# Performance work log

Hardware: AMD Instinct MI355X
Metric: run time of the kernel (lower is better)

The kernel has to match this reference:

```python
import jax, jax.numpy as jnp
import numpy as np


def _conv(x, w, b):
    # NCHW conv, SAME padding for odd kernel, stride 1
    pad = (w.shape[2] - 1) // 2
    y = jax.lax.conv_general_dilated(
        x, w, window_strides=(1, 1), padding=[(pad, pad), (pad, pad)],
        dimension_numbers=('NCHW', 'OIHW', 'NCHW'))
    return y + b[None, :, None, None]


def _cell(x, h, c, m, p):
    # one TransGRU cell step; x:[B,Cin,H,W], h/c/m:[B,hc,H,W]
    A = _conv(jnp.concatenate([x, h], axis=1), p['w_rzo'], p['b_rzo'])   # [B,3hc,H,W]
    Bm = _conv(jnp.concatenate([x, m], axis=1), p['w_rz'], p['b_rz'])    # [B,2hc,H,W]
    decay_h = jnp.exp(-p['td_h'])[None]          # (1,hc,1,1)
    decay_m = jnp.exp(-p['td_m'])[None]
    gate = jax.nn.sigmoid(p['tg'])[None]
    Ar, Az, Ao = jnp.split(A, 3, axis=1)
    Br, Bz = jnp.split(Bm, 2, axis=1)
    r = jax.nn.sigmoid(Ar * gate + h * decay_h)
    z = jax.nn.sigmoid(Az * gate + h * decay_h)
    o = jax.nn.sigmoid(Ao)
    xr = jax.nn.sigmoid(Br * gate + m * decay_m)
    xz = jax.nn.sigmoid(Bz * gate + m * decay_m)
    gc = jnp.tanh(_conv(jnp.concatenate([x, r * c], axis=1), p['w_h'], p['b_h']))
    gm = jnp.tanh(_conv(jnp.concatenate([x, xr * m], axis=1), p['w_h'], p['b_h']))
    c_new = z * c + (1 - z) * gc
    m_new = xz * m + (1 - xz) * gm
    h_new = o * jnp.tanh(_conv(jnp.concatenate([c_new, m_new], axis=1), p['w_o'], p['b_o']))
    return h_new, c_new, m_new, (r, z, xr, xz, c_new, m_new, gc, gm, o)


def _forward(x, params, attention_size):
    B, T, _, H, W = x.shape
    L = len(params)
    hcs = [p['w_rzo'].shape[0] // 3 for p in params]
    hc_last = hcs[-1]
    dtype = x.dtype
    init_states = tuple(
        tuple(jnp.zeros((B, hc, H, W), dtype) for _ in range(3)) for hc in hcs)
    init_gates = tuple(jnp.zeros((B, hc_last, H, W), dtype) for _ in range(9))

    def step(carry, xt):
        states, _ = carry
        inp = xt
        m = states[-1][2]  # layer 0 reads m from last layer of previous step
        new_states = []
        gates = None
        for l in range(L):
            h, c, _own_m = states[l]
            inp, cn, mn, gates = _cell(inp, h, c, m, params[l])
            new_states.append((inp, cn, mn))
            m = mn  # next layer reads m just produced by this layer
        return (tuple(new_states), gates), inp

    (final_states, gates), hs = jax.lax.scan(
        step, (init_states, init_gates), jnp.swapaxes(x, 0, 1))
    # gates from last layer at final step (matches torch leaking loop vars)
    r, z, xr, xz, c, m, gc, gm, o = gates
    q = ((r + xr + c + gc) * 0.25).reshape(B, hc_last, H * W)
    k = ((r + xr + m + gm) * 0.25).reshape(B, hc_last, H * W)
    v = jnp.swapaxes(hs, 0, 1).reshape(B, T, hc_last, H * W)
    scale = 1.0 / float(np.sqrt(attention_size))
    attn = jax.nn.softmax(jnp.einsum('bcn,bdn->bcd', q, k) * scale, axis=-1)
    out = jnp.einsum('bcd,btdn->btcn', attn, v).reshape(B, T, hc_last, H, W)
    return out


def setup_inputs() -> dict:
    key = jax.random.key(0)
    ks = jax.random.split(key, 32)
    d = {'x': jax.random.normal(ks[0], (4, 8, 16, 64, 64), jnp.float32)}
    specs = {
        'w_rzo0': (192, 80, 3, 3), 'b_rzo0': (192,), 'w_rz0': (128, 80, 3, 3),
        'b_rz0': (128,), 'w_h0': (64, 80, 3, 3), 'b_h0': (64,),
        'w_o0': (64, 128, 1, 1), 'b_o0': (64,), 'td_h0': (64, 1, 1),
        'td_m0': (64, 1, 1), 'tg0': (64, 1, 1),
        'w_rzo1': (192, 128, 3, 3), 'b_rzo1': (192,), 'w_rz1': (128, 128, 3, 3),
        'b_rz1': (128,), 'w_h1': (64, 128, 3, 3), 'b_h1': (64,),
        'w_o1': (64, 128, 1, 1), 'b_o1': (64,), 'td_h1': (64, 1, 1),
        'td_m1': (64, 1, 1), 'tg1': (64, 1, 1),
    }
    for i, (name, shp) in enumerate(specs.items()):
        d[name] = jax.random.normal(ks[i + 1], shp, jnp.float32) * 0.05
    d['attention_size'] = 4096
    return d


def reference(x, w_rzo0, b_rzo0, w_rz0, b_rz0, w_h0, b_h0, w_o0, b_o0,
              td_h0, td_m0, tg0, w_rzo1, b_rzo1, w_rz1, b_rz1, w_h1, b_h1,
              w_o1, b_o1, td_h1, td_m1, tg1, attention_size):
    params = [
        dict(w_rzo=w_rzo0, b_rzo=b_rzo0, w_rz=w_rz0, b_rz=b_rz0, w_h=w_h0,
             b_h=b_h0, w_o=w_o0, b_o=b_o0, td_h=td_h0, td_m=td_m0, tg=tg0),
        dict(w_rzo=w_rzo1, b_rzo=b_rzo1, w_rz=w_rz1, b_rz=b_rz1, w_h=w_h1,
             b_h=b_h1, w_o=w_o1, b_o=b_o1, td_h=td_h1, td_m=td_m1, tg=tg1),
    ]
    return _forward(x, params, attention_size)
```

## Files before the change

kernel.cpp:

```cpp
#include <hip/hip_runtime.h>
#include <math.h>

#define HWN 4096
#define Bn 4
#define Tn 8

typedef __attribute__((ext_vector_type(8))) _Float16 f16x8;
typedef __attribute__((ext_vector_type(4))) float floatx4;

__device__ __forceinline__ float sigmoidf_(float v) { return 1.f / (1.f + expf(-v)); }

__device__ __forceinline__ void split8(const float* vv, f16x8* hi, f16x8* lo) {
#pragma unroll
    for (int j = 0; j < 8; ++j) {
        _Float16 h = (_Float16)vv[j];
        (*hi)[j] = h;
        (*lo)[j] = (_Float16)(vv[j] - (float)h);
    }
}

__global__ __launch_bounds__(256) void prep_w_kernel(
    const float* __restrict__ W, _Float16* __restrict__ dst,
    int Ctot, int Cout, int nch, int KK)
{
    const int ncog = Cout >> 4;
    const long total = (long)KK * nch * ncog * 512;
    for (long i = (long)blockIdx.x * 256 + threadIdx.x; i < total;
         i += (long)gridDim.x * 256) {
        int j    = (int)(i & 7);
        int lane = (int)((i >> 3) & 63);
        long r   = i >> 9;
        int f = (int)(r % ncog); r /= ncog;
        int c = (int)(r % nch);  r /= nch;
        int kk = (int)r;
        int co = f * 16 + (lane & 15);
        int ci = c * 32 + (lane >> 4) * 8 + j;
        float v = (ci < Ctot) ? W[((long)co * Ctot + ci) * KK + kk] : 0.f;
        _Float16 hi = (_Float16)v;
        dst[i]         = hi;
        dst[total + i] = (_Float16)(v - (float)hi);
    }
}

__global__ __launch_bounds__(256) void prep_x_kernel(
    const float* __restrict__ x, float* __restrict__ xcl)
{
    const int i = blockIdx.x * 256 + threadIdx.x;
    const int px = i & 4095;
    const int t  = (i >> 12) & 7;
    const int b  = i >> 15;
    float* d = xcl + (((long)t * Bn + b) * HWN + px) * 16;
#pragma unroll
    for (int ch = 0; ch < 16; ++ch)
        d[ch] = x[((long)(b * 8 + t) * 16 + ch) * HWN + px];
}

template<int EPI, int NF>
__global__ __launch_bounds__(256) void conv3m(
    const float* __restrict__ in1, int C1,
    const float* __restrict__ in2a, const float* __restrict__ in2b,
    int Ctot, int nch,
    const _Float16* __restrict__ wA, const float* __restrict__ biasA,
    float* outA, int CoutA, int ncogA,
    const _Float16* __restrict__ wB, const float* __restrict__ biasB,
    float* outB, int CoutB, int ncogB, int nA,
    const float* zA, const float* zB,
    const float* sA, const float* sB,
    const float* rten, const float* xrten,
    float* qout, float* kout, int last)
{
    __shared__ __align__(16) _Float16 ldsB[18][18][2][40];

    const int tid = threadIdx.x;
    const int ty0 = (blockIdx.x >> 2) * 16;
    const int tx0 = (blockIdx.x & 3) * 16;
    const int b   = blockIdx.z & 3;
    const int which = (EPI == 1) ? (int)(blockIdx.z >> 2)
                                 : (blockIdx.y >= (unsigned)nA ? 1 : 0);

    const float*    in2  = which ? in2b : in2a;
    const _Float16* Wf   = which ? wB : wA;
    const float*    bias = which ? biasB : biasA;
    float*          outp = which ? outB : outA;
    const int Cout = which ? CoutB : CoutA;
    const int ncog = which ? ncogB : ncogA;
    const int cog0 = (EPI == 1) ? blockIdx.y * NF
                   : (which ? (blockIdx.y - nA) * NF : blockIdx.y * NF);
    const int co0  = cog0 * 16;

    const int lane = tid & 63, wv = tid >> 6, tl = lane & 15, quad = lane >> 4;
    const int C2 = Ctot - C1;
    const long wplane = (long)9 * nch * ncog * 512;
    const float* in1b  = in1 + (long)b * HWN * C1;
    const float* in2bb = in2 + (long)b * HWN * C2;

    floatx4 acc[NF][4];
#pragma unroll
    for (int f = 0; f < NF; ++f)
#pragma unroll
        for (int g = 0; g < 4; ++g) acc[f][g] = (floatx4){0.f, 0.f, 0.f, 0.f};

    float4 pa[6], pb[6];
    auto prefetch = [&](int c) {
        const int c0 = c * 32;
#pragma unroll
        for (int s = 0; s < 6; ++s) {
            const int i = tid + s * 256;
            float4 va = {0.f, 0.f, 0.f, 0.f}, vb = {0.f, 0.f, 0.f, 0.f};
            if (i < 1296) {
                const int pxh = i >> 2, cig = i & 3;
                const int yh = pxh / 18, xh = pxh - yh * 18;
                const int y = ty0 + yh - 1, x = tx0 + xh - 1;
                const int ch = c0 + cig * 8;
                if (ch < Ctot && (unsigned)y < 64u && (unsigned)x < 64u) {
                    const float* src; long off;
                    if (ch < C1) { src = in1b;  off = (long)(y * 64 + x) * C1 + ch; }
                    else         { src = in2bb; off = (long)(y * 64 + x) * C2 + ch - C1; }
                    va = *(const float4*)(src + off);
                    vb = *(const float4*)(src + off + 4);
                }
            }
            pa[s] = va; pb[s] = vb;
        }
    };

    prefetch(0);

    for (int c = 0; c < nch; ++c) {
        __syncthreads();
#pragma unroll
        for (int s = 0; s < 6; ++s) {
            const int i = tid + s * 256;
            if (i < 1296) {
                const int pxh = i >> 2, cig = i & 3;
                const int yh = pxh / 18, xh = pxh - yh * 18;
                float vv[8] = {pa[s].x, pa[s].y, pa[s].z, pa[s].w,
                               pb[s].x, pb[s].y, pb[s].z, pb[s].w};
                f16x8 vh, vl;
                split8(vv, &vh, &vl);
                *(f16x8*)&ldsB[yh][xh][0][cig * 8] = vh;
                *(f16x8*)&ldsB[yh][xh][1][cig * 8] = vl;
            }
        }
        __syncthreads();
        if (c + 1 < nch) prefetch(c + 1);

        f16x8 wh[2][NF], wl[2][NF];
        {
            const long wo0 = ((long)(0 * nch + c) * ncog + cog0) * 512 + lane * 8;
#pragma unroll
            for (int f = 0; f < NF; ++f) {
                wh[0][f] = *(const f16x8*)(Wf + wo0 + (long)f * 512);
                wl[0][f] = *(const f16x8*)(Wf + wplane + wo0 + (long)f * 512);
            }
        }
#pragma unroll
        for (int kk = 0; kk < 9; ++kk) {
            const int cur = kk & 1, nxt = cur ^ 1;
            if (kk < 8) {
                const long wo = ((long)((kk + 1) * nch + c) * ncog + cog0) * 512 + lane * 8;
#pragma unroll
                for (int f = 0; f < NF; ++f) {
                    wh[nxt][f] = *(const f16x8*)(Wf + wo + (long)f * 512);
                    wl[nxt][f] = *(const f16x8*)(Wf + wplane + wo + (long)f * 512);
                }
            }
            const int ky = kk / 3, kx = kk - ky * 3;
            f16x8 bh[4], bl[4];
#pragma unroll
            for (int g = 0; g < 4; ++g) {
                const _Float16* pB = &ldsB[wv * 4 + g + ky][tl + kx][0][quad * 8];
                bh[g] = *(const f16x8*)pB;
                bl[g] = *(const f16x8*)(pB + 40);
            }
#pragma unroll
            for (int f = 0; f < NF; ++f)
#pragma unroll
                for (int g = 0; g < 4; ++g) {
                    acc[f][g] = __builtin_amdgcn_mfma_f32_16x16x32_f16(wh[cur][f], bh[g], acc[f][g], 0, 0, 0);
                    acc[f][g] = __builtin_amdgcn_mfma_f32_16x16x32_f16(wh[cur][f], bl[g], acc[f][g], 0, 0, 0);
                    acc[f][g] = __builtin_amdgcn_mfma_f32_16x16x32_f16(wl[cur][f], bh[g], acc[f][g], 0, 0, 0);
                }
        }
    }

    if (EPI == 0) {
        const long obb = (long)b * HWN * Cout;
#pragma unroll
        for (int f = 0; f < NF; ++f) {
            const int co = co0 + f * 16 + quad * 4;
#pragma unroll
            for (int g = 0; g < 4; ++g) {
                const long px = (long)(ty0 + wv * 4 + g) * 64 + tx0 + tl;
                float4 v;
                v.x = acc[f][g][0] + bias[co + 0];
                v.y = acc[f][g][1] + bias[co + 1];
                v.z = acc[f][g][2] + bias[co + 2];
                v.w = acc[f][g][3] + bias[co + 3];
                *(float4*)(outp + obb + px * Cout + co) = v;
            }
        }
    } else {
        const float* zt = which ? zB : zA;
        const float* st = which ? sB : sA;
        float* qk = which ? kout : qout;
#pragma unroll
        for (int f = 0; f < NF; ++f) {
            const int co = co0 + f * 16 + quad * 4;
#pragma unroll
            for (int g = 0; g < 4; ++g) {
                const long px = (long)(ty0 + wv * 4 + g) * 64 + tx0 + tl;
                const long off = (long)b * HWN * 64 + px * 64 + co;
                float4 zv = *(const float4*)(zt + off);
                float4 sv = *(const float4*)(st + off);
                float gv[4], cn[4];
                gv[0] = tanhf(acc[f][g][0] + bias[co + 0]);
                gv[1] = tanhf(acc[f][g][1] + bias[co + 1]);
                gv[2] = tanhf(acc[f][g][2] + bias[co + 2]);
                gv[3] = tanhf(acc[f][g][3] + bias[co + 3]);
                cn[0] = zv.x * sv.x + (1.f - zv.x) * gv[0];
                cn[1] = zv.y * sv.y + (1.f - zv.y) * gv[1];
                cn[2] = zv.z * sv.z + (1.f - zv.z) * gv[2];
                cn[3] = zv.w * sv.w + (1.f - zv.w) * gv[3];
                *(float4*)(outp + off) = *(float4*)cn;
                if (last) {
                    float4 rv = *(const float4*)(rten + off);
                    float4 xv = *(const float4*)(xrten + off);
                    qk[((long)(b * 64) + co + 0) * HWN + px] = 0.25f * (rv.x + xv.x + cn[0] + gv[0]);
                    qk[((long)(b * 64) + co + 1) * HWN + px] = 0.25f * (rv.y + xv.y + cn[1] + gv[1]);
                    qk[((long)(b * 64) + co + 2) * HWN + px] = 0.25f * (rv.z + xv.z + cn[2] + gv[2]);
                    qk[((long)(b * 64) + co + 3) * HWN + px] = 0.25f * (rv.w + xv.w + cn[3] + gv[3]);
                }
            }
        }
    }
}

__global__ __launch_bounds__(256) void conv1x1m(
    const float* __restrict__ cten, const float* __restrict__ mten,
    const float* __restrict__ oten,
    const _Float16* __restrict__ W, const float* __restrict__ bias,
    float* houtp)
{
    const int tid = threadIdx.x;
    const int lane = tid & 63, wv = tid >> 6, tl = lane & 15, quad = lane >> 4;
    const int b = blockIdx.y;
    const int px = blockIdx.x * 64 + wv * 16 + tl;
    const long bb = (long)b * HWN * 64;

    f16x8 wh[4][4], wl[4][4];
#pragma unroll
    for (int c = 0; c < 4; ++c)
#pragma unroll
        for (int f = 0; f < 4; ++f) {
            const long wo = (long)(c * 4 + f) * 512 + lane * 8;
            wh[c][f] = *(const f16x8*)(W + wo);
            wl[c][f] = *(const f16x8*)(W + 8192 + wo);
        }
    f16x8 bh[4], bl[4];
#pragma unroll
    for (int c = 0; c < 4; ++c) {
        const float* src = (c < 2) ? cten : mten;
        const int ch0 = (c & 1) * 32 + quad * 8;
        const long off = bb + (long)px * 64 + ch0;
        float4 p0 = *(const float4*)(src + off);
        float4 p1 = *(const float4*)(src + off + 4);
        float vv[8] = {p0.x, p0.y, p0.z, p0.w, p1.x, p1.y, p1.z, p1.w};
        split8(vv, &bh[c], &bl[c]);
    }

    floatx4 acc[4];
#pragma unroll
    for (int f = 0; f < 4; ++f) acc[f] = (floatx4){0.f, 0.f, 0.f, 0.f};
#pragma unroll
    for (int c = 0; c < 4; ++c)
#pragma unroll
        for (int f = 0; f < 4; ++f) {
            acc[f] = __builtin_amdgcn_mfma_f32_16x16x32_f16(wh[c][f], bh[c], acc[f], 0, 0, 0);
            acc[f] = __builtin_amdgcn_mfma_f32_16x16x32_f16(wh[c][f], bl[c], acc[f], 0, 0, 0);
            acc[f] = __builtin_amdgcn_mfma_f32_16x16x32_f16(wl[c][f], bh[c], acc[f], 0, 0, 0);
        }

#pragma unroll
    for (int f = 0; f < 4; ++f) {
        const int co = f * 16 + quad * 4;
        const long off = bb + (long)px * 64 + co;
        float4 ov = *(const float4*)(oten + off);
        float4 hv;
        hv.x = ov.x * tanhf(acc[f][0] + bias[co + 0]);
        hv.y = ov.y * tanhf(acc[f][1] + bias[co + 1]);
        hv.z = ov.z * tanhf(acc[f][2] + bias[co + 2]);
        hv.w = ov.w * tanhf(acc[f][3] + bias[co + 3]);
        *(float4*)(houtp + off) = hv;
    }
}

__global__ __launch_bounds__(256) void gates_cl(
    const float* __restrict__ A, const float* __restrict__ Bm,
    const float* __restrict__ h, const float* __restrict__ m,
    const float* __restrict__ c,
    const float* __restrict__ td_h, const float* __restrict__ td_m,
    const float* __restrict__ tg,
    float* r, float* xr, float* z, float* xz,
    float* o, float* rc, float* xm)
{
    const int i  = blockIdx.x * 256 + threadIdx.x;
    const int ch = (i & 15) * 4;
    const long px = (i >> 4) & 4095;
    const int b  = i >> 16;
    const long b64  = ((long)b * HWN + px) * 64 + ch;
    const long b192 = ((long)b * HWN + px) * 192 + ch;
    const long b128 = ((long)b * HWN + px) * 128 + ch;

    float4 Ar = *(const float4*)(A + b192);
    float4 Az = *(const float4*)(A + b192 + 64);
    float4 Ao = *(const float4*)(A + b192 + 128);
    float4 Br = *(const float4*)(Bm + b128);
    float4 Bz = *(const float4*)(Bm + b128 + 64);
    float4 hv = *(const float4*)(h + b64);
    float4 mv = *(const float4*)(m + b64);
    float4 cv = *(const float4*)(c + b64);

    float rv[4], zv[4], ov[4], xrv[4], xzv[4], rcv[4], xmv[4];
    const float* Arp = (const float*)&Ar; const float* Azp = (const float*)&Az;
    const float* Aop = (const float*)&Ao; const float* Brp = (const float*)&Br;
    const float* Bzp = (const float*)&Bz; const float* hp = (const float*)&hv;
    const float* mp = (const float*)&mv;  const float* cp = (const float*)&cv;
#pragma unroll
    for (int j = 0; j < 4; ++j) {
        const float g  = sigmoidf_(tg[ch + j]);
        const float dh = expf(-td_h[ch + j]);
        const float dm = expf(-td_m[ch + j]);
        rv[j]  = sigmoidf_(Arp[j] * g + hp[j] * dh);
        zv[j]  = sigmoidf_(Azp[j] * g + hp[j] * dh);
        ov[j]  = sigmoidf_(Aop[j]);
        xrv[j] = sigmoidf_(Brp[j] * g + mp[j] * dm);
        xzv[j] = sigmoidf_(Bzp[j] * g + mp[j] * dm);
        rcv[j] = rv[j] * cp[j];
        xmv[j] = xrv[j] * mp[j];
    }
    *(float4*)(r  + b64) = *(float4*)rv;
    *(float4*)(xr + b64) = *(float4*)xrv;
    *(float4*)(z  + b64) = *(float4*)zv;
    *(float4*)(xz + b64) = *(float4*)xzv;
    *(float4*)(o  + b64) = *(float4*)ov;
    *(float4*)(rc + b64) = *(float4*)rcv;
    *(float4*)(xm + b64) = *(float4*)xmv;
}

__global__ __launch_bounds__(256) void logits_part(
    const float* __restrict__ q, const float* __restrict__ k, float* __restrict__ part)
{
    __shared__ float qs[64][66], ks[64][66];
    const int tid = threadIdx.x;
    const int b = blockIdx.x, kc = blockIdx.y;
    const int cqq = tid >> 4, ckq = tid & 15;
    float pacc[4][4];
#pragma unroll
    for (int u = 0; u < 4; ++u)
#pragma unroll
        for (int v = 0; v < 4; ++v) pacc[u][v] = 0.f;

    for (int sub = 0; sub < 4; ++sub) {
        const int px0 = kc * 256 + sub * 64;
        __syncthreads();
#pragma unroll
        for (int rr = 0; rr < 16; ++rr) {
            const int idx = rr * 256 + tid;
            const int chh = idx >> 6, pxo = idx & 63;
            qs[chh][pxo] = q[((long)b * 64 + chh) * HWN + px0 + pxo];
            ks[chh][pxo] = k[((long)b * 64 + chh) * HWN + px0 + pxo];
        }
        __syncthreads();
        for (int p = 0; p < 64; ++p) {
            float qv[4], kv[4];
#pragma unroll
            for (int u = 0; u < 4; ++u) { qv[u] = qs[cqq + 16 * u][p]; kv[u] = ks[ckq + 16 * u][p]; }
#pragma unroll
            for (int u = 0; u < 4; ++u)
#pragma unroll
                for (int v = 0; v < 4; ++v) pacc[u][v] = fmaf(qv[u], kv[v], pacc[u][v]);
        }
    }
#pragma unroll
    for (int u = 0; u < 4; ++u)
#pragma unroll
        for (int v = 0; v < 4; ++v)
            part[(((long)b * 16 + kc) * 64 + cqq + 16 * u) * 64 + ckq + 16 * v] = pacc[u][v];
}

__global__ void reduce_softmax(const float* __restrict__ part, float* __restrict__ attn)
{
    const int row = blockIdx.x;
    const int b = row >> 6, cq = row & 63;
    const int lane = threadIdx.x;
    float s = 0.f;
#pragma unroll
    for (int kc = 0; kc < 16; ++kc)
        s += part[(((long)b * 16 + kc) * 64 + cq) * 64 + lane];
    float v = s * (1.f / 64.f);
    float mx = v;
    for (int off = 32; off; off >>= 1) mx = fmaxf(mx, __shfl_xor(mx, off));
    float e = expf(v - mx);
    float sum = e;
    for (int off = 32; off; off >>= 1) sum += __shfl_xor(sum, off);
    attn[row * 64 + lane] = e / sum;
}

__global__ __launch_bounds__(256) void out_cl(
    const float* __restrict__ attn, const float* __restrict__ hs,
    float* __restrict__ outp)
{
    __shared__ __align__(16) float att_t[64][8];
    const int bt = blockIdx.x;
    const int b = bt >> 3, t = bt & 7;
    const int c0 = blockIdx.z * 8;
    const int tid = threadIdx.x;
    for (int i = tid; i < 512; i += 256) {
        int d = i >> 3, j = i & 7;
        att_t[d][j] = attn[(b * 64 + c0 + j) * 64 + d];
    }
    __syncthreads();

    const long px = blockIdx.y * 256 + tid;
    const long SLOT = (long)Bn * HWN * 64;
    const float* vb = hs + (long)t * SLOT + ((long)b * HWN + px) * 64;

    float acc[8];
#pragma unroll
    for (int j = 0; j < 8; ++j) acc[j] = 0.f;
#pragma unroll 4
    for (int dg = 0; dg < 16; ++dg) {
        float4 v4 = *(const float4*)(vb + dg * 4);
        const float* vp = (const float*)&v4;
#pragma unroll
        for (int j4 = 0; j4 < 4; ++j4) {
            const float vv = vp[j4];
            const float4 a0 = *(const float4*)&att_t[dg * 4 + j4][0];
            const float4 a1 = *(const float4*)&att_t[dg * 4 + j4][4];
            acc[0] = fmaf(vv, a0.x, acc[0]); acc[1] = fmaf(vv, a0.y, acc[1]);
            acc[2] = fmaf(vv, a0.z, acc[2]); acc[3] = fmaf(vv, a0.w, acc[3]);
            acc[4] = fmaf(vv, a1.x, acc[4]); acc[5] = fmaf(vv, a1.y, acc[5]);
            acc[6] = fmaf(vv, a1.z, acc[6]); acc[7] = fmaf(vv, a1.w, acc[7]);
        }
    }
    const long ob = ((long)(b * 8 + t) * 64 + c0) * HWN + px;
#pragma unroll
    for (int j = 0; j < 8; ++j) outp[ob + (long)j * HWN] = acc[j];
}

extern "C" void kernel_launch(void* const* d_in, const int* in_sizes, int n_in,
                              void* d_out, int out_size, void* d_ws, size_t ws_size,
                              hipStream_t stream)
{
    const float* x = (const float*)d_in[0];
    const float* w_rzo[2] = {(const float*)d_in[1],  (const float*)d_in[12]};
    const float* b_rzo[2] = {(const float*)d_in[2],  (const float*)d_in[13]};
    const float* w_rz[2]  = {(const float*)d_in[3],  (const float*)d_in[14]};
    const float* b_rz[2]  = {(const float*)d_in[4],  (const float*)d_in[15]};
    const float* w_h[2]   = {(const float*)d_in[5],  (const float*)d_in[16]};
    const float* b_h[2]   = {(const float*)d_in[6],  (const float*)d_in[17]};
    const float* w_o[2]   = {(const float*)d_in[7],  (const float*)d_in[18]};
    const float* b_o[2]   = {(const float*)d_in[8],  (const float*)d_in[19]};
    const float* td_h[2]  = {(const float*)d_in[9],  (const float*)d_in[20]};
    const float* td_m[2]  = {(const float*)d_in[10], (const float*)d_in[21]};
    const float* tg[2]    = {(const float*)d_in[11], (const float*)d_in[22]};

    const size_t S64 = (size_t)Bn * HWN * 64;
    float* P = (float*)d_ws;
    float* h0    = P; P += S64;
    float* c0    = P; P += S64;
    float* m0    = P; P += S64;
    float* c1    = P; P += S64;
    float* m1    = P; P += S64;
    float* zslab = P; P += S64;
    float* A_cl  = P; P += (size_t)Bn * HWN * 192;
    float* B_cl  = P; P += (size_t)Bn * HWN * 128;
    float* rb    = P; P += S64;
    float* xrb   = P; P += S64;
    float* zb    = P; P += S64;
    float* xzb   = P; P += S64;
    float* ogb   = P; P += S64;
    float* rcb   = P; P += S64;
    float* xmb   = P; P += S64;
    float* hs    = P; P += (size_t)Tn * S64;
    float* x_cl  = P; P += (size_t)Tn * Bn * HWN * 16;
    _Float16* wA0 = (_Float16*)P;
    _Float16* wB0 = wA0 + 331776;
    _Float16* wH0 = wB0 + 221184;
    _Float16* wA1 = wH0 + 110592;
    _Float16* wB1 = wA1 + 442368;
    _Float16* wH1 = wB1 + 294912;
    _Float16* wO0 = wH1 + 147456;
    _Float16* wO1 = wO0 + 16384;
    float* qbuf  = A_cl;
    float* kbuf  = qbuf + S64;
    float* partb = kbuf + S64;
    float* attnb = partb + (size_t)Bn * 16 * 64 * 64;

    hipMemsetAsync(h0, 0, 6 * S64 * sizeof(float), stream);

    prep_x_kernel<<<512, 256, 0, stream>>>(x, x_cl);
    prep_w_kernel<<<128, 256, 0, stream>>>(w_rzo[0], wA0, 80, 192, 3, 9);
    prep_w_kernel<<<128, 256, 0, stream>>>(w_rz[0],  wB0, 80, 128, 3, 9);
    prep_w_kernel<<<128, 256, 0, stream>>>(w_h[0],   wH0, 80,  64, 3, 9);
    prep_w_kernel<<<128, 256, 0, stream>>>(w_rzo[1], wA1, 128, 192, 4, 9);
    prep_w_kernel<<<128, 256, 0, stream>>>(w_rz[1],  wB1, 128, 128, 4, 9);
    prep_w_kernel<<<128, 256, 0, stream>>>(w_h[1],   wH1, 128, 64, 4, 9);
    prep_w_kernel<<<64, 256, 0, stream>>>(w_o[0], wO0, 128, 64, 4, 1);
    prep_w_kernel<<<64, 256, 0, stream>>>(w_o[1], wO1, 128, 64, 4, 1);

    for (int t = 0; t < Tn; ++t) {
        const float* xt = x_cl + (size_t)t * Bn * HWN * 16;
        const float* h1prev = (t == 0) ? zslab : (hs + (size_t)(t - 1) * S64);
        float* h1out = hs + (size_t)t * S64;

        conv3m<0, 2><<<dim3(16, 10, 4), 256, 0, stream>>>(
            xt, 16, h0, m1, 80, 3,
            wA0, b_rzo[0], A_cl, 192, 12,
            wB0, b_rz[0],  B_cl, 128, 8, 6,
            nullptr, nullptr, nullptr, nullptr, nullptr, nullptr, nullptr, nullptr, 0);
        gates_cl<<<1024, 256, 0, stream>>>(A_cl, B_cl, h0, m1, c0,
            td_h[0], td_m[0], tg[0], rb, xrb, zb, xzb, ogb, rcb, xmb);
        conv3m<1, 1><<<dim3(16, 4, 8), 256, 0, stream>>>(
            xt, 16, rcb, xmb, 80, 3,
            wH0, b_h[0], c0, 64, 4,
            wH0, b_h[0], m0, 64, 4, 0,
            zb, xzb, c0, m1, rb, xrb, qbuf, kbuf, 0);
        conv1x1m<<<dim3(64, 4), 256, 0, stream>>>(c0, m0, ogb, wO0, b_o[0], h0);

        conv3m<0, 2><<<dim3(16, 10, 4), 256, 0, stream>>>(
            h0, 64, h1prev, m0, 128, 4,
            wA1, b_rzo[1], A_cl, 192, 12,
            wB1, b_rz[1],  B_cl, 128, 8, 6,
            nullptr, nullptr, nullptr, nullptr, nullptr, nullptr, nullptr, nullptr, 0);
        gates_cl<<<1024, 256, 0, stream>>>(A_cl, B_cl, h1prev, m0, c1,
            td_h[1], td_m[1], tg[1], rb, xrb, zb, xzb, ogb, rcb, xmb);
        conv3m<1, 1><<<dim3(16, 4, 8), 256, 0, stream>>>(
            h0, 64, rcb, xmb, 128, 4,
            wH1, b_h[1], c1, 64, 4,
            wH1, b_h[1], m1, 64, 4, 0,
            zb, xzb, c1, m0, rb, xrb, qbuf, kbuf, (t == Tn - 1) ? 1 : 0);
        conv1x1m<<<dim3(64, 4), 256, 0, stream>>>(c1, m1, ogb, wO1, b_o[1], h1out);
    }

    logits_part<<<dim3(4, 16), 256, 0, stream>>>(qbuf, kbuf, partb);
    reduce_softmax<<<256, 64, 0, stream>>>(partb, attnb);
    out_cl<<<dim3(32, 16, 8), 256, 0, stream>>>(attnb, hs, (float*)d_out);
}
```

Measured before the change: 1.468 ms.

## Reshape conv tiles to more output channels and fewer rows per block

Adds a template parameter for the number of pixel rows per wave and retiles the 3x3 conv kernels. Each block now covers more output-channel groups (NF=4) over fewer spatial rows (NG=2 or 1), which gives more weight reuse per LDS tile and changes the grid shape. It also drops the register prefetch of the next channel chunk in favour of a direct load-split-store loop, and reorders the MFMA issue into three separate passes. The trade-off is a larger halo fraction per tile, no more overlap of global loads with compute, and different register pressure and occupancy.

```diff
diff --git a/kernel.cpp b/kernel.cpp
--- a/kernel.cpp
+++ b/kernel.cpp
@@ -55,7 +55,7 @@
         d[ch] = x[((long)(b * 8 + t) * 16 + ch) * HWN + px];
 }
 
-template<int EPI, int NF>
+template<int EPI, int NF, int NG>
 __global__ __launch_bounds__(256) void conv3m(
     const float* __restrict__ in1, int C1,
     const float* __restrict__ in2a, const float* __restrict__ in2b,
@@ -69,10 +69,10 @@
     const float* rten, const float* xrten,
     float* qout, float* kout, int last)
 {
-    __shared__ __align__(16) _Float16 ldsB[18][18][2][40];
+    __shared__ __align__(16) _Float16 ldsB[4 * NG + 2][18][2][40];
 
     const int tid = threadIdx.x;
-    const int ty0 = (blockIdx.x >> 2) * 16;
+    const int ty0 = (blockIdx.x >> 2) * (4 * NG);
     const int tx0 = (blockIdx.x & 3) * 16;
     const int b   = blockIdx.z & 3;
     const int which = (EPI == 1) ? (int)(blockIdx.z >> 2)
@@ -94,56 +94,37 @@
     const float* in1b  = in1 + (long)b * HWN * C1;
     const float* in2bb = in2 + (long)b * HWN * C2;
 
-    floatx4 acc[NF][4];
+    floatx4 acc[NF][NG];
 #pragma unroll
     for (int f = 0; f < NF; ++f)
 #pragma unroll
-        for (int g = 0; g < 4; ++g) acc[f][g] = (floatx4){0.f, 0.f, 0.f, 0.f};
-
-    float4 pa[6], pb[6];
-    auto prefetch = [&](int c) {
-        const int c0 = c * 32;
-#pragma unroll
-        for (int s = 0; s < 6; ++s) {
-            const int i = tid + s * 256;
-            float4 va = {0.f, 0.f, 0.f, 0.f}, vb = {0.f, 0.f, 0.f, 0.f};
-            if (i < 1296) {
-                const int pxh = i >> 2, cig = i & 3;
-                const int yh = pxh / 18, xh = pxh - yh * 18;
-                const int y = ty0 + yh - 1, x = tx0 + xh - 1;
-                const int ch = c0 + cig * 8;
-                if (ch < Ctot && (unsigned)y < 64u && (unsigned)x < 64u) {
-                    const float* src; long off;
-                    if (ch < C1) { src = in1b;  off = (long)(y * 64 + x) * C1 + ch; }
-                    else         { src = in2bb; off = (long)(y * 64 + x) * C2 + ch - C1; }
-                    va = *(const float4*)(src + off);
-                    vb = *(const float4*)(src + off + 4);
-                }
-            }
-            pa[s] = va; pb[s] = vb;
-        }
-    };
-
-    prefetch(0);
+        for (int g = 0; g < NG; ++g) acc[f][g] = (floatx4){0.f, 0.f, 0.f, 0.f};
+
+    const int UNITS = (4 * NG + 2) * 18 * 4;
 
     for (int c = 0; c < nch; ++c) {
         __syncthreads();
-#pragma unroll
-        for (int s = 0; s < 6; ++s) {
-            const int i = tid + s * 256;
-            if (i < 1296) {
-                const int pxh = i >> 2, cig = i & 3;
-                const int yh = pxh / 18, xh = pxh - yh * 18;
-                float vv[8] = {pa[s].x, pa[s].y, pa[s].z, pa[s].w,
-                               pb[s].x, pb[s].y, pb[s].z, pb[s].w};
-                f16x8 vh, vl;
+        const int c0 = c * 32;
+        for (int i = tid; i < UNITS; i += 256) {
+            const int pxh = i >> 2, cig = i & 3;
+            const int yh = pxh / 18, xh = pxh - yh * 18;
+            const int y = ty0 + yh - 1, x = tx0 + xh - 1;
+            const int ch = c0 + cig * 8;
+            f16x8 vh = {0, 0, 0, 0, 0, 0, 0, 0};
+            f16x8 vl = {0, 0, 0, 0, 0, 0, 0, 0};
+            if (ch < Ctot && (unsigned)y < 64u && (unsigned)x < 64u) {
+                const float* src; long off;
+                if (ch < C1) { src = in1b;  off = (long)(y * 64 + x) * C1 + ch; }
+                else         { src = in2bb; off = (long)(y * 64 + x) * C2 + ch - C1; }
+                float4 a  = *(const float4*)(src + off);
+                float4 b4 = *(const float4*)(src + off + 4);
+                float vv[8] = {a.x, a.y, a.z, a.w, b4.x, b4.y, b4.z, b4.w};
                 split8(vv, &vh, &vl);
-                *(f16x8*)&ldsB[yh][xh][0][cig * 8] = vh;
-                *(f16x8*)&ldsB[yh][xh][1][cig * 8] = vl;
             }
+            *(f16x8*)&ldsB[yh][xh][0][cig * 8] = vh;
+            *(f16x8*)&ldsB[yh][xh][1][cig * 8] = vl;
         }
         __syncthreads();
-        if (c + 1 < nch) prefetch(c + 1);
 
         f16x8 wh[2][NF], wl[2][NF];
         {
@@ -166,21 +147,28 @@
                 }
             }
             const int ky = kk / 3, kx = kk - ky * 3;
-            f16x8 bh[4], bl[4];
-#pragma unroll
-            for (int g = 0; g < 4; ++g) {
-                const _Float16* pB = &ldsB[wv * 4 + g + ky][tl + kx][0][quad * 8];
+            f16x8 bh[NG], bl[NG];
+#pragma unroll
+            for (int g = 0; g < NG; ++g) {
+                const _Float16* pB = &ldsB[wv * NG + g + ky][tl + kx][0][quad * 8];
                 bh[g] = *(const f16x8*)pB;
                 bl[g] = *(const f16x8*)(pB + 40);
             }
 #pragma unroll
             for (int f = 0; f < NF; ++f)
 #pragma unroll
-                for (int g = 0; g < 4; ++g) {
+                for (int g = 0; g < NG; ++g)
                     acc[f][g] = __builtin_amdgcn_mfma_f32_16x16x32_f16(wh[cur][f], bh[g], acc[f][g], 0, 0, 0);
+#pragma unroll
+            for (int f = 0; f < NF; ++f)
+#pragma unroll
+                for (int g = 0; g < NG; ++g)
                     acc[f][g] = __builtin_amdgcn_mfma_f32_16x16x32_f16(wh[cur][f], bl[g], acc[f][g], 0, 0, 0);
+#pragma unroll
+            for (int f = 0; f < NF; ++f)
+#pragma unroll
+                for (int g = 0; g < NG; ++g)
                     acc[f][g] = __builtin_amdgcn_mfma_f32_16x16x32_f16(wl[cur][f], bh[g], acc[f][g], 0, 0, 0);
-                }
         }
     }
 
@@ -190,8 +178,8 @@
         for (int f = 0; f < NF; ++f) {
             const int co = co0 + f * 16 + quad * 4;
 #pragma unroll
-            for (int g = 0; g < 4; ++g) {
-                const long px = (long)(ty0 + wv * 4 + g) * 64 + tx0 + tl;
+            for (int g = 0; g < NG; ++g) {
+                const long px = (long)(ty0 + wv * NG + g) * 64 + tx0 + tl;
                 float4 v;
                 v.x = acc[f][g][0] + bias[co + 0];
                 v.y = acc[f][g][1] + bias[co + 1];
@@ -208,8 +196,8 @@
         for (int f = 0; f < NF; ++f) {
             const int co = co0 + f * 16 + quad * 4;
 #pragma unroll
-            for (int g = 0; g < 4; ++g) {
-                const long px = (long)(ty0 + wv * 4 + g) * 64 + tx0 + tl;
+            for (int g = 0; g < NG; ++g) {
+                const long px = (long)(ty0 + wv * NG + g) * 64 + tx0 + tl;
                 const long off = (long)b * HWN * 64 + px * 64 + co;
                 float4 zv = *(const float4*)(zt + off);
                 float4 sv = *(const float4*)(st + off);
@@ -515,28 +503,28 @@
         const float* h1prev = (t == 0) ? zslab : (hs + (size_t)(t - 1) * S64);
         float* h1out = hs + (size_t)t * S64;
 
-        conv3m<0, 2><<<dim3(16, 10, 4), 256, 0, stream>>>(
+        conv3m<0, 4, 2><<<dim3(32, 5, 4), 256, 0, stream>>>(
             xt, 16, h0, m1, 80, 3,
             wA0, b_rzo[0], A_cl, 192, 12,
-            wB0, b_rz[0],  B_cl, 128, 8, 6,
+            wB0, b_rz[0],  B_cl, 128, 8, 3,
             nullptr, nullptr, nullptr, nullptr, nullptr, nullptr, nullptr, nullptr, 0);
         gates_cl<<<1024, 256, 0, stream>>>(A_cl, B_cl, h0, m1, c0,
             td_h[0], td_m[0], tg[0], rb, xrb, zb, xzb, ogb, rcb, xmb);
-        conv3m<1, 1><<<dim3(16, 4, 8), 256, 0, stream>>>(
+        conv3m<1, 4, 1><<<dim3(64, 1, 8), 256, 0, stream>>>(
             xt, 16, rcb, xmb, 80, 3,
             wH0, b_h[0], c0, 64, 4,
             wH0, b_h[0], m0, 64, 4, 0,
             zb, xzb, c0, m1, rb, xrb, qbuf, kbuf, 0);
         conv1x1m<<<dim3(64, 4), 256, 0, stream>>>(c0, m0, ogb, wO0, b_o[0], h0);
 
-        conv3m<0, 2><<<dim3(16, 10, 4), 256, 0, stream>>>(
+        conv3m<0, 4, 2><<<dim3(32, 5, 4), 256, 0, stream>>>(
             h0, 64, h1prev, m0, 128, 4,
             wA1, b_rzo[1], A_cl, 192, 12,
-            wB1, b_rz[1],  B_cl, 128, 8, 6,
+            wB1, b_rz[1],  B_cl, 128, 8, 3,
             nullptr, nullptr, nullptr, nullptr, nullptr, nullptr, nullptr, nullptr, 0);
         gates_cl<<<1024, 256, 0, stream>>>(A_cl, B_cl, h1prev, m0, c1,
             td_h[1], td_m[1], tg[1], rb, xrb, zb, xzb, ogb, rcb, xmb);
-        conv3m<1, 1><<<dim3(16, 4, 8), 256, 0, stream>>>(
+        conv3m<1, 4, 1><<<dim3(64, 1, 8), 256, 0, stream>>>(
             h0, 64, rcb, xmb, 128, 4,
             wH1, b_h[1], c1, 64, 4,
             wH1, b_h[1], m1, 64, 4, 0,
```

New measurement: 1.564 ms. 6.5% more time.
